# Performance work log

Measured on AMD Instinct MI355X. Metric: run time of the kernel, lower is better.

The kernel has to match this reference:

```python
import jax, jax.numpy as jnp
import numpy as np

B, S, D, E = 4, 1024, 1024, 4
HID = 2816  # multiple_of * ceil(int(2*4*D/3) / multiple_of), multiple_of=256
COND = 1024  # min(D, 1024)
NORM_EPS = 1e-5  # block norms
LN_EPS = 1e-5    # q_norm/k_norm default eps


def setup_inputs() -> dict:
    key = jax.random.key(0)
    ks = jax.random.split(key, 16)
    w = lambda i, shape: jax.random.normal(ks[i], shape, jnp.float32) * 0.02
    return {
        'x': jax.random.normal(ks[0], (B, S, D), jnp.float32),
        'freqs_cis': jax.random.normal(ks[1], (S, 32), jnp.float32),  # unused by the block
        'adaln_input': jax.random.normal(ks[2], (B, COND), jnp.float32),
        'wq': w(3, (D, D)), 'wk': w(4, (D, D)), 'wv': w(5, (D, D)), 'wo': w(6, (D, D)),
        'q_norm_w': jnp.ones((D,), jnp.float32), 'q_norm_b': jnp.zeros((D,), jnp.float32),
        'k_norm_w': jnp.ones((D,), jnp.float32), 'k_norm_b': jnp.zeros((D,), jnp.float32),
        'attn_norm_w': jnp.ones((D,), jnp.float32), 'attn_norm_b': jnp.zeros((D,), jnp.float32),
        'ffn_norm_w': jnp.ones((D,), jnp.float32), 'ffn_norm_b': jnp.zeros((D,), jnp.float32),
        'w1': w(7, (E, D, HID)), 'w2': w(8, (E, HID, D)), 'w3': w(9, (E, D, HID)),
        'router_w': w(10, (D, E)), 'router_b': jnp.zeros((E,), jnp.float32),
        'ada_w': w(11, (COND, 6 * D)), 'ada_b': jnp.zeros((6 * D,), jnp.float32),
    }


def _ln(x, w, b, eps):
    mu = jnp.mean(x, -1, keepdims=True)
    var = jnp.mean((x - mu) ** 2, -1, keepdims=True)
    return (x - mu) * jax.lax.rsqrt(var + eps) * w + b


def _attention(x, wq, wk, wv, wo, qn_w, qn_b, kn_w, kn_b):
    # NOTE: this module attends over the FEATURE dim (no head split, no 1/sqrt(d) scale):
    # xq,xk,xv are permuted to [B, D, S]; scores are [B, D, D].
    q = _ln(x @ wq, qn_w, qn_b, LN_EPS)
    k = _ln(x @ wk, kn_w, kn_b, LN_EPS)
    v = x @ wv
    scores = jnp.einsum('bsd,bse->bde', q, k)          # [B, D, D]
    attn = jax.nn.softmax(scores, axis=-1)
    out = jnp.einsum('bde,bse->bsd', attn, v)          # [B, S, D]
    return out @ wo


def _moe(x, w1, w2, w3, router_w, router_b):
    logits = x @ router_w + router_b                   # [B, S, E]
    # F.normalize default dim=1 -> L2-normalize along the SEQUENCE dim (faithful quirk)
    nrm = jnp.sqrt(jnp.sum(logits * logits, axis=1, keepdims=True))
    logits = logits / jnp.maximum(nrm, 1e-12)
    probs = jax.nn.softmax(logits, axis=-1)
    topw, topi = jax.lax.top_k(probs, 2)
    # dense combine weights [B,S,E]: identical math to the masked gather/scatter dispatch
    combine = jnp.sum(jax.nn.one_hot(topi, E, dtype=x.dtype) * topw[..., None], axis=-2)
    h1 = jnp.einsum('bsd,edh->ebsh', x, w1)
    h3 = jnp.einsum('bsd,edh->ebsh', x, w3)
    out_e = jnp.einsum('ebsh,ehd->ebsd', jnp.sin(h1) * h3, w2)
    moe = jnp.einsum('bse,ebsd->bsd', combine, out_e)
    avg = jnp.mean(probs, axis=0)                      # [S, E] (mean over batch dim only)
    aux = jnp.sum((1.0 / E - avg) ** 2)
    return moe, aux


def reference(x, freqs_cis, adaln_input, wq, wk, wv, wo, q_norm_w, q_norm_b, k_norm_w,
              k_norm_b, attn_norm_w, attn_norm_b, ffn_norm_w, ffn_norm_b, w1, w2, w3,
              router_w, router_b, ada_w, ada_b):
    ada = jax.nn.silu(adaln_input) @ ada_w + ada_b     # [B, 6D]
    shift_msa, scale_msa, gate_msa, shift_mlp, scale_mlp, gate_mlp = jnp.split(ada, 6, axis=1)
    h = _ln(x, attn_norm_w, attn_norm_b, NORM_EPS)
    h = h * (1.0 + scale_msa[:, None, :]) + shift_msa[:, None, :]
    x = x + gate_msa[:, None, :] * _attention(h, wq, wk, wv, wo, q_norm_w, q_norm_b, k_norm_w, k_norm_b)
    h = _ln(x, ffn_norm_w, ffn_norm_b, NORM_EPS)
    h = h * (1.0 + scale_mlp[:, None, :]) + shift_mlp[:, None, :]
    # MoE path REPLACES x (no residual, gate_mlp unused) — faithful to the source
    x, aux = _moe(h, w1, w2, w3, router_w, router_b)
    return x, aux
```

## Files before the change

kernel.cpp:

```cpp
#include <hip/hip_runtime.h>
#include <hip/hip_bf16.h>
#include <math.h>

#define BB 4
#define SS 1024
#define DD 1024
#define EE 4
#define HID 2816
#define HC 1408
#define SIXD 6144
#define NSLOT 8704
#define NMB 68

typedef __bf16 v8bf __attribute__((ext_vector_type(8)));
typedef float  v4f  __attribute__((ext_vector_type(4)));

__device__ __forceinline__ ushort f2bf(float f) {
    union { float f; unsigned u; } v; v.f = f;
    unsigned r = v.u + 0x7fff + ((v.u >> 16) & 1);
    return (ushort)(r >> 16);
}
__device__ __forceinline__ float bf2f(ushort u) {
    union { unsigned u; float f; } v; v.u = ((unsigned)u) << 16;
    return v.f;
}
__device__ __forceinline__ void split_bf(float x, ushort& h, ushort& l) {
    h = f2bf(x);
    l = f2bf(x - bf2f(h));
}
__device__ __forceinline__ void gload16(const void* g, void* l) {
    __builtin_amdgcn_global_load_lds((const __attribute__((address_space(1))) void*)g,
                                     (__attribute__((address_space(3))) void*)l, 16, 0, 0);
}
template<int N> __device__ __forceinline__ void wait_vm() {
    __builtin_amdgcn_s_waitcnt((N & 15) | (0x7 << 4) | (0xF << 8) | ((N >> 4) << 14));
}

__device__ __forceinline__ void xcd_remap(int& bx, int& by) {
    const int gx = gridDim.x, gy = gridDim.y;
    const int nwg = gx * gy;
    const int wid = bx + gx * by;
    const int q = nwg >> 3, r = nwg & 7;
    const int xcd = wid & 7, loc = wid >> 3;
    const int pos = (xcd < r) ? (xcd * (q + 1) + loc)
                              : (r * (q + 1) + (xcd - r) * q + loc);
    bx = pos % gx; by = pos / gx;
}

__device__ __forceinline__ void moe_remap(int& bx, int& by) {
    const int gx = gridDim.x, gy = gridDim.y;
    const int total = gx * gy;
    const int wid = bx + gx * by;
    if ((total & 7) || (gx & 1)) { xcd_remap(bx, by); return; }
    const int q = total >> 3;
    const int pos = (wid & 7) * q + (wid >> 3);
    const int NG = gx >> 1;
    const int gh = NG * gy;
    const int nh = pos / gh, r = pos % gh;
    by = r / NG;
    bx = nh * NG + (r % NG);
}

template<int EPI, bool SPLIT, bool MOE>
__global__ __launch_bounds__(256, 2) void mgemm(
    const ushort* __restrict__ Ah, const ushort* __restrict__ Al,
    const ushort* __restrict__ Bh, const ushort* __restrict__ Bl,
    void* __restrict__ Cv, ushort* __restrict__ C2,
    const float* __restrict__ f1, const float* __restrict__ f2,
    const int* __restrict__ tokidx, const int* __restrict__ mbe,
    const int* __restrict__ mbm,
    int K, int lda, int ldb, int ldc,
    long sA, long sB, long sC)
{
    constexpr int STG = SPLIT ? 12288 : 6144;
    constexpr int BH  = SPLIT ? 8192 : 4096;
    constexpr int L   = SPLIT ? 6 : 3;
    constexpr int NST = SPLIT ? 2 : 3;
    __shared__ __align__(16) ushort smem[NST * STG];

    const int tid  = threadIdx.x;
    const int wv   = tid >> 6, lane = tid & 63;

    int bx = blockIdx.x, by = blockIdx.y;
    if (MOE) moe_remap(bx, by); else xcd_remap(bx, by);
    const int n0 = bx * 64;

    int eexp = 0, m0;
    if (MOE) {
        eexp = mbe[by];
        if (eexp < 0) return;
        m0 = mbm[by];
    } else {
        m0 = by * 128;
    }
    const long zA = MOE ? 0 : (long)blockIdx.z * sA;
    const long zB = MOE ? (long)eexp * sB : (long)blockIdx.z * sB;
    const long zC = MOE ? 0 : (long)blockIdx.z * sC;

    const int lrow = tid >> 2;
    const int skq  = ((tid & 3) ^ ((tid >> 3) & 3)) * 8;
    const int lm   = lane & 15;
    const int qs   = (((lane >> 4) ^ ((lm >> 1) & 3)) * 8);

    v4f acc[2][4];
    const v4f vzero = {0.f, 0.f, 0.f, 0.f};
    #pragma unroll
    for (int i = 0; i < 2; ++i)
        #pragma unroll
        for (int j = 0; j < 4; ++j) acc[i][j] = vzero;

    auto issue = [&](int kt, int st) {
        const long kk = (long)kt * 32 + skq;
        ushort* base = smem + st * STG;
        #pragma unroll
        for (int c = 0; c < 2; ++c) {
            const int row  = c * 64 + lrow;
            const int loff = (c * 64 + wv * 16) * 32;
            gload16(Ah + zA + (long)(m0 + row) * lda + kk, base + loff);
            if (SPLIT)
                gload16(Al + zA + (long)(m0 + row) * lda + kk, base + 4096 + loff);
        }
        {
            const int loff = wv * 16 * 32;
            gload16(Bh + zB + (long)(n0 + lrow) * ldb + kk, base + BH + loff);
            if (SPLIT)
                gload16(Bl + zB + (long)(n0 + lrow) * ldb + kk, base + BH + 2048 + loff);
        }
    };

    const int nk = K / 32;
    issue(0, 0);
    if (!SPLIT && nk > 1) issue(1, 1);
    for (int kt = 0; kt < nk; ++kt) {
        const int stg = SPLIT ? (kt & 1) : (kt % 3);
        if (SPLIT) {
            if (kt) __builtin_amdgcn_s_barrier();
            const bool hasNext = (kt + 1 < nk);
            if (hasNext) issue(kt + 1, stg ^ 1);
            if (hasNext) wait_vm<L>(); else wait_vm<0>();
            __builtin_amdgcn_s_barrier();
        } else {
            if (kt + 1 < nk) wait_vm<L>(); else wait_vm<0>();
            __builtin_amdgcn_s_barrier();
            if (kt + 2 < nk) issue(kt + 2, (kt + 2) % 3);
        }
        const ushort* As = smem + stg * STG;
        v8bf a[2], b[4];
        #pragma unroll
        for (int i = 0; i < 2; ++i) a[i] = *(const v8bf*)(As + (wv*32 + 16*i + lm) * 32 + qs);
        #pragma unroll
        for (int j = 0; j < 4; ++j) b[j] = *(const v8bf*)(As + BH + (16*j + lm) * 32 + qs);
        #pragma unroll
        for (int i = 0; i < 2; ++i)
            #pragma unroll
            for (int j = 0; j < 4; ++j)
                acc[i][j] = __builtin_amdgcn_mfma_f32_16x16x32_bf16(a[i], b[j], acc[i][j], 0, 0, 0);
        if (SPLIT) {
            v8bf al[2], bl[4];
            #pragma unroll
            for (int i = 0; i < 2; ++i) al[i] = *(const v8bf*)(As + 4096 + (wv*32 + 16*i + lm) * 32 + qs);
            #pragma unroll
            for (int j = 0; j < 4; ++j) bl[j] = *(const v8bf*)(As + BH + 2048 + (16*j + lm) * 32 + qs);
            #pragma unroll
            for (int i = 0; i < 2; ++i)
                #pragma unroll
                for (int j = 0; j < 4; ++j) {
                    acc[i][j] = __builtin_amdgcn_mfma_f32_16x16x32_bf16(a[i],  bl[j], acc[i][j], 0, 0, 0);
                    acc[i][j] = __builtin_amdgcn_mfma_f32_16x16x32_bf16(al[i], b[j],  acc[i][j], 0, 0, 0);
                }
        }
    }

    const int r0 = (lane >> 4) * 4;
    if (EPI == 7) {
        #pragma unroll
        for (int i = 0; i < 2; ++i)
            #pragma unroll
            for (int r = 0; r < 4; ++r) {
                const int rowg = m0 + wv*32 + 16*i + r0 + r;
                const int t = tokidx[rowg];
                if (t >= 0) {
                    const float cw = f1[t * 4 + eexp];
                    #pragma unroll
                    for (int j = 0; j < 4; ++j)
                        atomicAdd((float*)Cv + (long)t * 1024 + n0 + 16*j + lm, cw * acc[i][j][r]);
                }
            }
    } else {
        #pragma unroll
        for (int i = 0; i < 2; ++i) {
            #pragma unroll
            for (int j = 0; j < 4; ++j) {
                const int colg = n0 + 16*j + lm;
                #pragma unroll
                for (int r = 0; r < 4; ++r) {
                    const long rowg = (long)(m0 + wv*32 + 16*i + r0 + r);
                    const long idx  = zC + rowg * ldc + colg;
                    const float val = acc[i][j][r];
                    if (EPI == 0) {
                        ((float*)Cv)[idx] = val;
                    } else if (EPI == 2) {
                        ((float*)Cv)[idx] = f1[idx] + f2[(rowg >> 10) * SIXD + 2048 + colg] * val;
                    } else if (EPI == 5) {
                        ushort h, l; split_bf(val, h, l);
                        ((ushort*)Cv)[idx] = h;
                        C2[idx] = l;
                    }
                }
            }
        }
    }
}

__global__ __launch_bounds__(256, 2) void mgemm_h1h3(
    const ushort* __restrict__ Ah, const ushort* __restrict__ B1,
    const ushort* __restrict__ B2, ushort* __restrict__ Cb,
    const int* __restrict__ tokidx, const int* __restrict__ mbe,
    const int* __restrict__ mbm, long sB)
{
    constexpr int STG = 8192;
    __shared__ __align__(16) ushort smem[3 * STG];

    const int tid  = threadIdx.x;
    const int wv   = tid >> 6, lane = tid & 63;

    int bx = blockIdx.x, by = blockIdx.y;
    moe_remap(bx, by);
    const int n0 = bx * 64;
    const int eexp = mbe[by];
    if (eexp < 0) return;
    const int m0 = mbm[by];
    const long zB = (long)eexp * sB;

    const int lrow = tid >> 2;
    const int skq  = ((tid & 3) ^ ((tid >> 3) & 3)) * 8;
    const int lm   = lane & 15;
    const int qs   = (((lane >> 4) ^ ((lm >> 1) & 3)) * 8);

    long arow[2];
    #pragma unroll
    for (int c = 0; c < 2; ++c) {
        const int t = tokidx[m0 + c * 64 + lrow];
        arow[c] = (t < 0) ? 0 : (long)t;
    }

    v4f acc[2][4], acc2[2][4];
    const v4f vzero = {0.f, 0.f, 0.f, 0.f};
    #pragma unroll
    for (int i = 0; i < 2; ++i)
        #pragma unroll
        for (int j = 0; j < 4; ++j) { acc[i][j] = vzero; acc2[i][j] = vzero; }

    auto issue = [&](int kt, int st) {
        const long kk = (long)kt * 32 + skq;
        ushort* base = smem + st * STG;
        #pragma unroll
        for (int c = 0; c < 2; ++c)
            gload16(Ah + arow[c] * 1024 + kk, base + (c * 64 + wv * 16) * 32);
        const int loff = wv * 16 * 32;
        gload16(B1 + zB + (long)(n0 + lrow) * 1024 + kk, base + 4096 + loff);
        gload16(B2 + zB + (long)(n0 + lrow) * 1024 + kk, base + 6144 + loff);
    };

    issue(0, 0);
    issue(1, 1);
    for (int kt = 0; kt < 32; ++kt) {
        if (kt + 1 < 32) wait_vm<4>(); else wait_vm<0>();
        __builtin_amdgcn_s_barrier();
        if (kt + 2 < 32) issue(kt + 2, (kt + 2) % 3);
        const ushort* As = smem + (kt % 3) * STG;
        v8bf a[2], b1[4], b2[4];
        #pragma unroll
        for (int i = 0; i < 2; ++i) a[i] = *(const v8bf*)(As + (wv*32 + 16*i + lm) * 32 + qs);
        #pragma unroll
        for (int j = 0; j < 4; ++j) {
            b1[j] = *(const v8bf*)(As + 4096 + (16*j + lm) * 32 + qs);
            b2[j] = *(const v8bf*)(As + 6144 + (16*j + lm) * 32 + qs);
        }
        #pragma unroll
        for (int i = 0; i < 2; ++i)
            #pragma unroll
            for (int j = 0; j < 4; ++j) {
                acc[i][j]  = __builtin_amdgcn_mfma_f32_16x16x32_bf16(a[i], b1[j], acc[i][j],  0, 0, 0);
                acc2[i][j] = __builtin_amdgcn_mfma_f32_16x16x32_bf16(a[i], b2[j], acc2[i][j], 0, 0, 0);
            }
    }

    const int r0 = (lane >> 4) * 4;
    #pragma unroll
    for (int i = 0; i < 2; ++i)
        #pragma unroll
        for (int j = 0; j < 4; ++j) {
            const int colg = n0 + 16*j + lm;
            #pragma unroll
            for (int r = 0; r < 4; ++r) {
                const long rowg = (long)(m0 + wv*32 + 16*i + r0 + r);
                Cb[rowg * HC + colg] = f2bf(sinf(acc[i][j][r]) * acc2[i][j][r]);
            }
        }
}

template<bool SP>
__global__ __launch_bounds__(256) void transp(
    const float* __restrict__ in, ushort* __restrict__ oh, ushort* __restrict__ ol,
    int ldin, int ldout, long sIn, long sOut)
{
    __shared__ float T[64][65];
    const int n0 = blockIdx.x * 64, k0 = blockIdx.y * 64;
    in += (long)blockIdx.z * sIn;
    oh += (long)blockIdx.z * sOut;
    if (SP) ol += (long)blockIdx.z * sOut;
    const int t = threadIdx.x;
    const int rr = t >> 4, c4 = (t & 15) * 4;
    #pragma unroll
    for (int p = 0; p < 4; ++p) {
        const int r = rr + p * 16;
        const float4 v = *(const float4*)(in + (long)(k0 + r) * ldin + n0 + c4);
        T[c4+0][r] = v.x; T[c4+1][r] = v.y; T[c4+2][r] = v.z; T[c4+3][r] = v.w;
    }
    __syncthreads();
    #pragma unroll
    for (int p = 0; p < 4; ++p) {
        const int idx = t + 256 * p;
        const int n = idx >> 4, c = (idx & 15) * 4;
        ushort4 wh, wl;
        float x0 = T[n][c], x1 = T[n][c+1], x2 = T[n][c+2], x3 = T[n][c+3];
        if (SP) {
            split_bf(x0, wh.x, wl.x); split_bf(x1, wh.y, wl.y);
            split_bf(x2, wh.z, wl.z); split_bf(x3, wh.w, wl.w);
        } else {
            wh.x = f2bf(x0); wh.y = f2bf(x1); wh.z = f2bf(x2); wh.w = f2bf(x3);
        }
        *(ushort4*)(oh + (long)(n0 + n) * ldout + k0 + c) = wh;
        if (SP) *(ushort4*)(ol + (long)(n0 + n) * ldout + k0 + c) = wl;
    }
}

__global__ __launch_bounds__(256) void ada_kernel(
    const float* __restrict__ adaln, const float* __restrict__ aw,
    const float* __restrict__ ab, float* __restrict__ ada)
{
    __shared__ float s[DD];
    const int b = blockIdx.y;
    const int tid = threadIdx.x;
    for (int i = tid; i < DD; i += 256) {
        const float v = adaln[(long)b * DD + i];
        s[i] = v / (1.f + expf(-v));
    }
    __syncthreads();
    const int n = blockIdx.x * 256 + tid;
    float acc = 0.f;
    for (int k = 0; k < DD; ++k) acc += s[k] * aw[(long)k * SIXD + n];
    ada[(long)b * SIXD + n] = acc + ab[n];
}

template<int OUT, bool MOD>
__global__ __launch_bounds__(256) void ln_kernel(
    const float* __restrict__ x, const float* __restrict__ w, const float* __restrict__ bias,
    const float* __restrict__ ada, int scale_off, int shift_off,
    float* __restrict__ o32, ushort* __restrict__ oh, ushort* __restrict__ ol, float eps)
{
    const int row = blockIdx.x;
    const int b = row >> 10;
    const int tid = threadIdx.x;
    const float* xr = x + (long)row * DD;
    float v[4]; float s = 0.f, q = 0.f;
    #pragma unroll
    for (int i = 0; i < 4; ++i) { v[i] = xr[tid + 256*i]; s += v[i]; q += v[i]*v[i]; }
    __shared__ float rs_[256], rq_[256];
    rs_[tid] = s; rq_[tid] = q; __syncthreads();
    for (int off = 128; off > 0; off >>= 1) {
        if (tid < off) { rs_[tid] += rs_[tid+off]; rq_[tid] += rq_[tid+off]; }
        __syncthreads();
    }
    const float mu  = rs_[0] * (1.f/DD);
    const float var = rq_[0] * (1.f/DD) - mu*mu;
    const float rstd = rsqrtf(var + eps);
    const float* ar = ada + (long)b * SIXD;
    #pragma unroll
    for (int i = 0; i < 4; ++i) {
        const int d = tid + 256*i;
        float y = (v[i] - mu) * rstd * w[d] + bias[d];
        if (MOD) y = y * (1.f + ar[scale_off + d]) + ar[shift_off + d];
        const long idx = (long)row * DD + d;
        if (OUT == 0) o32[idx] = y;
        else if (OUT == 1) { ushort h, l; split_bf(y, h, l); oh[idx] = h; ol[idx] = l; }
        else oh[idx] = f2bf(y);
    }
}

__global__ __launch_bounds__(256) void softmax_split(
    const float* __restrict__ in, ushort* __restrict__ oh, ushort* __restrict__ ol)
{
    const long row = blockIdx.x;
    const float* p = in + row * 1024;
    const int tid = threadIdx.x;
    float v[4]; float mx = -INFINITY;
    #pragma unroll
    for (int i = 0; i < 4; ++i) { v[i] = p[tid + 256*i]; mx = fmaxf(mx, v[i]); }
    __shared__ float red[256];
    red[tid] = mx; __syncthreads();
    for (int off = 128; off > 0; off >>= 1) {
        if (tid < off) red[tid] = fmaxf(red[tid], red[tid+off]);
        __syncthreads();
    }
    const float rowmax = red[0];
    __syncthreads();
    float s = 0.f;
    #pragma unroll
    for (int i = 0; i < 4; ++i) { v[i] = expf(v[i] - rowmax); s += v[i]; }
    red[tid] = s; __syncthreads();
    for (int off = 128; off > 0; off >>= 1) {
        if (tid < off) red[tid] += red[tid+off];
        __syncthreads();
    }
    const float inv = 1.f / red[0];
    #pragma unroll
    for (int i = 0; i < 4; ++i) {
        ushort h, l; split_bf(v[i] * inv, h, l);
        oh[row*1024 + tid + 256*i] = h;
        ol[row*1024 + tid + 256*i] = l;
    }
}

__global__ __launch_bounds__(256) void router_fused(
    const float* __restrict__ x2, const float* __restrict__ fw, const float* __restrict__ fb,
    const float* __restrict__ ada, const float* __restrict__ rw, const float* __restrict__ rb,
    float* __restrict__ logits)
{
    const int row = blockIdx.x;
    const int b = row >> 10;
    const int tid = threadIdx.x;
    const float* xr = x2 + (long)row * DD;
    float v[4]; float s = 0.f, q = 0.f;
    #pragma unroll
    for (int i = 0; i < 4; ++i) { v[i] = xr[tid + 256*i]; s += v[i]; q += v[i]*v[i]; }
    __shared__ float rs_[256], rq_[256];
    rs_[tid] = s; rq_[tid] = q; __syncthreads();
    for (int off = 128; off > 0; off >>= 1) {
        if (tid < off) { rs_[tid] += rs_[tid+off]; rq_[tid] += rq_[tid+off]; }
        __syncthreads();
    }
    const float mu  = rs_[0] * (1.f/DD);
    const float var = rq_[0] * (1.f/DD) - mu*mu;
    const float rstd = rsqrtf(var + 1e-5f);
    const float* ar = ada + (long)b * SIXD;
    float acc[4] = {0.f, 0.f, 0.f, 0.f};
    #pragma unroll
    for (int i = 0; i < 4; ++i) {
        const int d = tid + 256*i;
        float h = (v[i] - mu) * rstd * fw[d] + fb[d];
        h = h * (1.f + ar[4096 + d]) + ar[3072 + d];
        const float* r4 = rw + (long)d * 4;
        acc[0] += h*r4[0]; acc[1] += h*r4[1]; acc[2] += h*r4[2]; acc[3] += h*r4[3];
    }
    __syncthreads();
    __shared__ float red[256];
    for (int e = 0; e < EE; ++e) {
        red[tid] = acc[e]; __syncthreads();
        for (int off = 128; off > 0; off >>= 1) {
            if (tid < off) red[tid] += red[tid+off];
            __syncthreads();
        }
        if (tid == 0) logits[(long)row * EE + e] = red[0] + rb[e];
        __syncthreads();
    }
}

__global__ __launch_bounds__(1024) void router_all(
    const float* __restrict__ logits, float* __restrict__ comb,
    float* __restrict__ auxout, int* __restrict__ tokidx,
    int* __restrict__ mbe, int* __restrict__ mbm)
{
    __shared__ float pl[16384];
    __shared__ float red[1024];
    __shared__ float nrm_l[16];
    __shared__ int lc[4], loff[4], lpos[4];
    const int tid = threadIdx.x;
    const int wv = tid >> 6, ln = tid & 63;
    {
        const int b = wv >> 2, e = wv & 3;
        float s = 0.f;
        for (int it = 0; it < 16; ++it) {
            const float v = logits[(((long)b << 10) + ln + (it << 6)) * 4 + e];
            s += v * v;
        }
        for (int off = 32; off > 0; off >>= 1) s += __shfl_down(s, off, 64);
        if (ln == 0) nrm_l[wv] = fmaxf(sqrtf(s), 1e-12f);
    }
    if (tid < 4) lc[tid] = 0;
    __syncthreads();
    float cloc[4][4];
    const int rbase = tid * 4;
    for (int rr = 0; rr < 4; ++rr) {
        const int row = rbase + rr;
        const int b = row >> 10;
        float l[4], p[4];
        #pragma unroll
        for (int e = 0; e < 4; ++e) l[e] = logits[(long)row*4 + e] / nrm_l[b*4 + e];
        const float mx = fmaxf(fmaxf(l[0], l[1]), fmaxf(l[2], l[3]));
        float s = 0.f;
        #pragma unroll
        for (int e = 0; e < 4; ++e) { p[e] = expf(l[e] - mx); s += p[e]; }
        const float inv = 1.f / s;
        #pragma unroll
        for (int e = 0; e < 4; ++e) { p[e] *= inv; pl[row*4 + e] = p[e]; }
        int i1 = 0;
        #pragma unroll
        for (int e = 1; e < 4; ++e) if (p[e] > p[i1]) i1 = e;
        int i2 = (i1 == 0) ? 1 : 0;
        #pragma unroll
        for (int e = 0; e < 4; ++e) if (e != i1 && p[e] > p[i2]) i2 = e;
        #pragma unroll
        for (int e = 0; e < 4; ++e) {
            const float c = (e == i1) ? p[i1] : ((e == i2) ? p[i2] : 0.f);
            cloc[rr][e] = c;
            comb[(long)row*4 + e] = c;
            if (c > 0.f) atomicAdd(&lc[e], 1);
        }
    }
    __syncthreads();
    float acc = 0.f;
    for (int i = tid; i < 4096; i += 1024) {
        const int s = i >> 2, e = i & 3;
        const float avg = 0.25f * (pl[s*4+e] + pl[(1024+s)*4+e] +
                                   pl[(2048+s)*4+e] + pl[(3072+s)*4+e]);
        const float d = 0.25f - avg;
        acc += d * d;
    }
    red[tid] = acc; __syncthreads();
    for (int off = 512; off > 0; off >>= 1) {
        if (tid < off) red[tid] += red[tid+off];
        __syncthreads();
    }
    if (tid == 0) auxout[0] = red[0];
    if (tid == 0) {
        int off0 = 0, nb = 0;
        for (int e = 0; e < 4; ++e) {
            loff[e] = off0; lpos[e] = 0;
            const int mb = (lc[e] + 127) >> 7;
            for (int k = 0; k < mb; ++k) { mbe[nb] = e; mbm[nb] = off0 + k*128; ++nb; }
            off0 += mb << 7;
        }
        for (; nb < NMB; ++nb) { mbe[nb] = -1; mbm[nb] = 0; }
    }
    for (int i = tid; i < NSLOT; i += 1024) tokidx[i] = -1;
    __syncthreads();
    for (int rr = 0; rr < 4; ++rr) {
        const int row = rbase + rr;
        #pragma unroll
        for (int e = 0; e < 4; ++e)
            if (cloc[rr][e] > 0.f) {
                const int s = atomicAdd(&lpos[e], 1);
                tokidx[loff[e] + s] = row;
            }
    }
}

__global__ __launch_bounds__(256) void zero_kernel(float4* __restrict__ out)
{
    out[(long)blockIdx.x * 256 + threadIdx.x] = float4{0.f, 0.f, 0.f, 0.f};
}

extern "C" void kernel_launch(void* const* d_in, const int* in_sizes, int n_in,
                              void* d_out, int out_size, void* d_ws, size_t ws_size,
                              hipStream_t stream)
{
    (void)in_sizes; (void)n_in; (void)out_size; (void)ws_size;
    const float* x     = (const float*)d_in[0];
    const float* adaln = (const float*)d_in[2];
    const float* wq    = (const float*)d_in[3];
    const float* wk    = (const float*)d_in[4];
    const float* wv    = (const float*)d_in[5];
    const float* wo    = (const float*)d_in[6];
    const float* qn_w  = (const float*)d_in[7];
    const float* qn_b  = (const float*)d_in[8];
    const float* kn_w  = (const float*)d_in[9];
    const float* kn_b  = (const float*)d_in[10];
    const float* an_w  = (const float*)d_in[11];
    const float* an_b  = (const float*)d_in[12];
    const float* fn_w  = (const float*)d_in[13];
    const float* fn_b  = (const float*)d_in[14];
    const float* w1    = (const float*)d_in[15];
    const float* w2    = (const float*)d_in[16];
    const float* w3    = (const float*)d_in[17];
    const float* rw    = (const float*)d_in[18];
    const float* rb    = (const float*)d_in[19];
    const float* aw    = (const float*)d_in[20];
    const float* ab    = (const float*)d_in[21];
    float* out = (float*)d_out;

    const long NBAT = (long)SS * DD;
    const long NBUF = (long)BB * SS * DD;
#define MB(x) ((long)(x) * 1048576L)

    char* P = (char*)d_ws;
    float* ada    = (float*)P;
    float* logits = (float*)(P + 98304);
    float* comb   = logits + 16384;
    int*   tokidx = (int*)(comb + 16384);
    int*   mbe    = tokidx + NSLOT;
    int*   mbm    = mbe + NMB;

    char* A0 = P + MB(1);
    ushort* wqT_h = (ushort*)(A0 + MB(0));  ushort* wqT_l = (ushort*)(A0 + MB(2));
    ushort* wkT_h = (ushort*)(A0 + MB(4));  ushort* wkT_l = (ushort*)(A0 + MB(6));
    ushort* wvT_h = (ushort*)(A0 + MB(8));  ushort* wvT_l = (ushort*)(A0 + MB(10));
    ushort* woT_h = (ushort*)(A0 + MB(0));  ushort* woT_l = (ushort*)(A0 + MB(2));
    ushort* w1Tc  = (ushort*)(A0 + MB(0));
    ushort* h_h  = (ushort*)(A0 + MB(12));  ushort* h_l  = (ushort*)(A0 + MB(20));
    float*  sc   = (float*) (A0 + MB(12));
    ushort* ao_h = (ushort*)(A0 + MB(12));  ushort* ao_l = (ushort*)(A0 + MB(20));
    ushort* actb = (ushort*)(A0 + MB(12));
    float*  qk32 = (float*) (A0 + MB(28));
    ushort* at_h = (ushort*)(A0 + MB(28));  ushort* at_l = (ushort*)(A0 + MB(36));
    ushort* v_h  = (ushort*)(A0 + MB(44));  ushort* v_l  = (ushort*)(A0 + MB(52));
    ushort* qT_h = (ushort*)(A0 + MB(60));  ushort* qT_l = (ushort*)(A0 + MB(68));
    float*  x2   = (float*) (A0 + MB(60));
    ushort* w3Tc = (ushort*)(A0 + MB(60));
    ushort* kT_h = (ushort*)(A0 + MB(76));  ushort* kT_l = (ushort*)(A0 + MB(84));
    ushort* h2bf = (ushort*)(A0 + MB(76));
    ushort* w2Tc = (ushort*)(A0 + MB(84));

    const dim3 blk(256);

    ada_kernel<<<dim3(SIXD/256, BB), blk, 0, stream>>>(adaln, aw, ab, ada);

    transp<true><<<dim3(16,16,1), blk, 0, stream>>>(wq, wqT_h, wqT_l, 1024, 1024, 0, 0);
    transp<true><<<dim3(16,16,1), blk, 0, stream>>>(wk, wkT_h, wkT_l, 1024, 1024, 0, 0);
    transp<true><<<dim3(16,16,1), blk, 0, stream>>>(wv, wvT_h, wvT_l, 1024, 1024, 0, 0);

    ln_kernel<1,true><<<4096, blk, 0, stream>>>(x, an_w, an_b, ada, 1024, 0,
                                                nullptr, h_h, h_l, 1e-5f);

    mgemm<0,true,false><<<dim3(16,32,1), blk, 0, stream>>>(
        h_h, h_l, wqT_h, wqT_l, qk32, nullptr, nullptr, nullptr, nullptr, nullptr, nullptr,
        1024, 1024, 1024, 1024, 0, 0, 0);
    ln_kernel<0,false><<<4096, blk, 0, stream>>>(qk32, qn_w, qn_b, ada, 0, 0, qk32, nullptr, nullptr, 1e-5f);
    transp<true><<<dim3(16,16,BB), blk, 0, stream>>>(qk32, qT_h, qT_l, 1024, 1024, NBAT, NBAT);

    mgemm<0,true,false><<<dim3(16,32,1), blk, 0, stream>>>(
        h_h, h_l, wkT_h, wkT_l, qk32, nullptr, nullptr, nullptr, nullptr, nullptr, nullptr,
        1024, 1024, 1024, 1024, 0, 0, 0);
    ln_kernel<0,false><<<4096, blk, 0, stream>>>(qk32, kn_w, kn_b, ada, 0, 0, qk32, nullptr, nullptr, 1e-5f);
    transp<true><<<dim3(16,16,BB), blk, 0, stream>>>(qk32, kT_h, kT_l, 1024, 1024, NBAT, NBAT);

    mgemm<5,true,false><<<dim3(16,32,1), blk, 0, stream>>>(
        h_h, h_l, wvT_h, wvT_l, v_h, v_l, nullptr, nullptr, nullptr, nullptr, nullptr,
        1024, 1024, 1024, 1024, 0, 0, 0);

    transp<true><<<dim3(16,16,1), blk, 0, stream>>>(wo, woT_h, woT_l, 1024, 1024, 0, 0);

    mgemm<0,true,false><<<dim3(16,8,BB), blk, 0, stream>>>(
        qT_h, qT_l, kT_h, kT_l, sc, nullptr, nullptr, nullptr, nullptr, nullptr, nullptr,
        1024, 1024, 1024, 1024, NBAT, NBAT, NBAT);

    softmax_split<<<4096, blk, 0, stream>>>(sc, at_h, at_l);

    mgemm<5,true,false><<<dim3(16,8,BB), blk, 0, stream>>>(
        v_h, v_l, at_h, at_l, ao_h, ao_l, nullptr, nullptr, nullptr, nullptr, nullptr,
        1024, 1024, 1024, 1024, NBAT, NBAT, NBAT);

    mgemm<2,true,false><<<dim3(16,32,1), blk, 0, stream>>>(
        ao_h, ao_l, woT_h, woT_l, x2, nullptr, x, ada, nullptr, nullptr, nullptr,
        1024, 1024, 1024, 1024, 0, 0, 0);

    ln_kernel<2,true><<<4096, blk, 0, stream>>>(x2, fn_w, fn_b, ada, 4096, 3072,
                                                nullptr, h2bf, nullptr, 1e-5f);

    router_fused<<<4096, blk, 0, stream>>>(x2, fn_w, fn_b, ada, rw, rb, logits);
    router_all<<<1, dim3(1024), 0, stream>>>(logits, comb, out + NBUF, tokidx, mbe, mbm);
    zero_kernel<<<dim3(4096), blk, 0, stream>>>((float4*)out);

    for (int c = 0; c < HID/HC; ++c) {
        transp<false><<<dim3(22,16,4), blk, 0, stream>>>(
            w1 + (long)c*HC, w1Tc, nullptr, HID, 1024, (long)DD*HID, (long)HC*1024);
        transp<false><<<dim3(22,16,4), blk, 0, stream>>>(
            w3 + (long)c*HC, w3Tc, nullptr, HID, 1024, (long)DD*HID, (long)HC*1024);
        transp<false><<<dim3(16,22,4), blk, 0, stream>>>(
            w2 + (long)c*HC*DD, w2Tc, nullptr, DD, HC, (long)HID*DD, (long)DD*HC);
        mgemm_h1h3<<<dim3(22, NMB), blk, 0, stream>>>(
            h2bf, w1Tc, w3Tc, actb, tokidx, mbe, mbm, (long)HC*1024);
        mgemm<7,false,true><<<dim3(16, NMB), blk, 0, stream>>>(
            actb, nullptr, w2Tc, nullptr, out, nullptr, comb, nullptr, tokidx, mbe, mbm,
            HC, HC, HC, 1024, 0, (long)DD*HC, 0);
    }
#undef MB
}
```

Measured before the change: 818.5 us.

## Widen MoE h1/h3 GEMM tile to 128x128 with 512-thread blocks

The fused w1/w3 expert GEMM now uses 8 waves per block in a 2x4 layout and covers 128 columns per block instead of 64, halving the grid in x. Each A tile is reused across twice as many B columns, which cuts global reads of the gathered activations. The block-to-XCD remap also switches to a column-major variant so blocks sharing a column of weights land on the same XCD. In exchange, LDS per block grows to about 72 KB, which may limit occupancy, and the grid has fewer blocks to spread over the CUs.

```diff
diff --git a/kernel.cpp b/kernel.cpp
--- a/kernel.cpp
+++ b/kernel.cpp
@@ -45,6 +45,17 @@
     const int pos = (xcd < r) ? (xcd * (q + 1) + loc)
                               : (r * (q + 1) + (xcd - r) * q + loc);
     bx = pos % gx; by = pos / gx;
+}
+
+__device__ __forceinline__ void xcd_remap_cm(int& bx, int& by) {
+    const int gx = gridDim.x, gy = gridDim.y;
+    const int nwg = gx * gy;
+    const int wid = bx + gx * by;
+    const int q = nwg >> 3, r = nwg & 7;
+    const int xcd = wid & 7, loc = wid >> 3;
+    const int pos = (xcd < r) ? (xcd * (q + 1) + loc)
+                              : (r * (q + 1) + (xcd - r) * q + loc);
+    bx = pos / gy; by = pos % gy;
 }
 
 __device__ __forceinline__ void moe_remap(int& bx, int& by) {
@@ -212,21 +223,22 @@
     }
 }
 
-__global__ __launch_bounds__(256, 2) void mgemm_h1h3(
+__global__ __launch_bounds__(512, 2) void mgemm_h1h3(
     const ushort* __restrict__ Ah, const ushort* __restrict__ B1,
     const ushort* __restrict__ B2, ushort* __restrict__ Cb,
     const int* __restrict__ tokidx, const int* __restrict__ mbe,
     const int* __restrict__ mbm, long sB)
 {
-    constexpr int STG = 8192;
+    constexpr int STG = 12288;
     __shared__ __align__(16) ushort smem[3 * STG];
 
     const int tid  = threadIdx.x;
     const int wv   = tid >> 6, lane = tid & 63;
+    const int wr   = wv >> 2, wc = wv & 3;
 
     int bx = blockIdx.x, by = blockIdx.y;
-    moe_remap(bx, by);
-    const int n0 = bx * 64;
+    xcd_remap_cm(bx, by);
+    const int n0 = bx * 128;
     const int eexp = mbe[by];
     if (eexp < 0) return;
     const int m0 = mbm[by];
@@ -237,64 +249,62 @@
     const int lm   = lane & 15;
     const int qs   = (((lane >> 4) ^ ((lm >> 1) & 3)) * 8);
 
-    long arow[2];
-    #pragma unroll
-    for (int c = 0; c < 2; ++c) {
-        const int t = tokidx[m0 + c * 64 + lrow];
-        arow[c] = (t < 0) ? 0 : (long)t;
-    }
-
-    v4f acc[2][4], acc2[2][4];
+    const int t = tokidx[m0 + lrow];
+    const long arow = (t < 0) ? 0 : (long)t;
+
+    v4f acc[4][2], acc2[4][2];
     const v4f vzero = {0.f, 0.f, 0.f, 0.f};
     #pragma unroll
-    for (int i = 0; i < 2; ++i)
-        #pragma unroll
-        for (int j = 0; j < 4; ++j) { acc[i][j] = vzero; acc2[i][j] = vzero; }
+    for (int i = 0; i < 4; ++i)
+        #pragma unroll
+        for (int j = 0; j < 2; ++j) { acc[i][j] = vzero; acc2[i][j] = vzero; }
 
     auto issue = [&](int kt, int st) {
         const long kk = (long)kt * 32 + skq;
         ushort* base = smem + st * STG;
-        #pragma unroll
-        for (int c = 0; c < 2; ++c)
-            gload16(Ah + arow[c] * 1024 + kk, base + (c * 64 + wv * 16) * 32);
         const int loff = wv * 16 * 32;
+        gload16(Ah + arow * 1024 + kk, base + loff);
         gload16(B1 + zB + (long)(n0 + lrow) * 1024 + kk, base + 4096 + loff);
-        gload16(B2 + zB + (long)(n0 + lrow) * 1024 + kk, base + 6144 + loff);
+        gload16(B2 + zB + (long)(n0 + lrow) * 1024 + kk, base + 8192 + loff);
     };
 
     issue(0, 0);
     issue(1, 1);
+    int s_cur = 0, s_nxt = 2;
+    #pragma unroll 1
     for (int kt = 0; kt < 32; ++kt) {
-        if (kt + 1 < 32) wait_vm<4>(); else wait_vm<0>();
+        if (kt + 1 < 32) wait_vm<3>(); else wait_vm<0>();
         __builtin_amdgcn_s_barrier();
-        if (kt + 2 < 32) issue(kt + 2, (kt + 2) % 3);
-        const ushort* As = smem + (kt % 3) * STG;
-        v8bf a[2], b1[4], b2[4];
-        #pragma unroll
-        for (int i = 0; i < 2; ++i) a[i] = *(const v8bf*)(As + (wv*32 + 16*i + lm) * 32 + qs);
-        #pragma unroll
-        for (int j = 0; j < 4; ++j) {
-            b1[j] = *(const v8bf*)(As + 4096 + (16*j + lm) * 32 + qs);
-            b2[j] = *(const v8bf*)(As + 6144 + (16*j + lm) * 32 + qs);
-        }
-        #pragma unroll
-        for (int i = 0; i < 2; ++i)
-            #pragma unroll
-            for (int j = 0; j < 4; ++j) {
+        if (kt + 2 < 32) issue(kt + 2, s_nxt);
+        const ushort* As = smem + s_cur * STG;
+        v8bf a[4], b1[2], b2[2];
+        #pragma unroll
+        for (int i = 0; i < 4; ++i) a[i] = *(const v8bf*)(As + (wr*64 + 16*i + lm) * 32 + qs);
+        #pragma unroll
+        for (int j = 0; j < 2; ++j) {
+            b1[j] = *(const v8bf*)(As + 4096 + (wc*32 + 16*j + lm) * 32 + qs);
+            b2[j] = *(const v8bf*)(As + 8192 + (wc*32 + 16*j + lm) * 32 + qs);
+        }
+        #pragma unroll
+        for (int i = 0; i < 4; ++i)
+            #pragma unroll
+            for (int j = 0; j < 2; ++j) {
                 acc[i][j]  = __builtin_amdgcn_mfma_f32_16x16x32_bf16(a[i], b1[j], acc[i][j],  0, 0, 0);
                 acc2[i][j] = __builtin_amdgcn_mfma_f32_16x16x32_bf16(a[i], b2[j], acc2[i][j], 0, 0, 0);
             }
+        s_cur = (s_cur == 2) ? 0 : s_cur + 1;
+        s_nxt = (s_nxt == 2) ? 0 : s_nxt + 1;
     }
 
     const int r0 = (lane >> 4) * 4;
     #pragma unroll
-    for (int i = 0; i < 2; ++i)
-        #pragma unroll
-        for (int j = 0; j < 4; ++j) {
-            const int colg = n0 + 16*j + lm;
+    for (int i = 0; i < 4; ++i)
+        #pragma unroll
+        for (int j = 0; j < 2; ++j) {
+            const int colg = n0 + wc*32 + 16*j + lm;
             #pragma unroll
             for (int r = 0; r < 4; ++r) {
-                const long rowg = (long)(m0 + wv*32 + 16*i + r0 + r);
+                const long rowg = (long)(m0 + wr*64 + 16*i + r0 + r);
                 Cb[rowg * HC + colg] = f2bf(sinf(acc[i][j][r]) * acc2[i][j][r]);
             }
         }
@@ -679,7 +689,7 @@
             w3 + (long)c*HC, w3Tc, nullptr, HID, 1024, (long)DD*HID, (long)HC*1024);
         transp<false><<<dim3(16,22,4), blk, 0, stream>>>(
             w2 + (long)c*HC*DD, w2Tc, nullptr, DD, HC, (long)HID*DD, (long)DD*HC);
-        mgemm_h1h3<<<dim3(22, NMB), blk, 0, stream>>>(
+        mgemm_h1h3<<<dim3(11, NMB), dim3(512), 0, stream>>>(
             h2bf, w1Tc, w3Tc, actb, tokidx, mbe, mbm, (long)HC*1024);
         mgemm<7,false,true><<<dim3(16, NMB), blk, 0, stream>>>(
             actb, nullptr, w2Tc, nullptr, out, nullptr, comb, nullptr, tokidx, mbe, mbm,
```

Result: no change. 833.0 us (+1.8%).
